# Kernel tuning notes

Hardware: AMD Instinct MI355X
Metric: run time of the kernel (lower is better)

The kernel has to match this reference:

```python
import jax, jax.numpy as jnp
import numpy as np

QMIN, QMAX = 0.0, 255.0  # uint8 affine quantization range


def _quant_dequant(x, scale, zero_point):
    # affine static quantization: q = clamp(round(x/scale) + zp, 0, 255)
    q = jnp.clip(jnp.round(x / scale) + zero_point, QMIN, QMAX)
    # dequantize back to float for the reference GEMM
    return (q - zero_point) * scale


def setup_inputs() -> dict:
    key = jax.random.key(0)
    k1, k2, k3, k4, k5 = jax.random.split(key, 5)
    N, IN, OUT = 4096, 4096, 4096
    x = jax.random.normal(k1, (N, IN), dtype=jnp.float32)
    weight = jax.random.normal(k2, (OUT, IN), dtype=jnp.float32) * 0.02
    bias = jax.random.normal(k3, (OUT,), dtype=jnp.float32)
    # static qparams (as produced by calculate_qparams of the observers)
    act_scale = jnp.float32(4.0 * 2.0 / 255.0)  # covers ~[-4, 4]
    act_zero_point = jnp.int32(128)
    weight_scale = (jax.random.uniform(k4, (OUT,), dtype=jnp.float32) * 0.5 + 0.5) * (0.08 * 2.0 / 255.0)
    weight_zero_point = jnp.full((OUT,), 128, dtype=jnp.int32)
    return {
        "x": x,
        "weight": weight,
        "bias": bias,
        "act_scale": act_scale,
        "act_zero_point": act_zero_point,
        "weight_scale": weight_scale,
        "weight_zero_point": weight_zero_point,
    }


def reference(x, weight, bias, act_scale, act_zero_point, weight_scale, weight_zero_point):
    # per-tensor static activation quantization
    x_dq = _quant_dequant(x, act_scale, act_zero_point.astype(jnp.float32))  # [N, in]
    # per-output-row weight quantization (block_size = (1, in_features))
    w_dq = _quant_dequant(
        weight,
        weight_scale[:, None],
        weight_zero_point.astype(jnp.float32)[:, None],
    )  # [out, in]
    # F.linear: x @ W^T + b
    return jnp.einsum("ni,oi->no", x_dq, w_dq) + bias
```

## Files before the change

kernel.cpp:

```cpp
#include <hip/hip_runtime.h>
#include <stdint.h>

typedef int   int4v   __attribute__((ext_vector_type(4)));
typedef float float4v __attribute__((ext_vector_type(4)));

static constexpr int DIM = 4096;
static constexpr int BM  = 256, BN = 256;
static constexpr int BK  = 128;
static constexpr int NKT = DIM / BK;

__global__ __launch_bounds__(256) void quant_act_kernel(
    const float* __restrict__ x, const float* __restrict__ s_ptr,
    const int* __restrict__ zp_ptr, int* __restrict__ out, int n4) {
  const float s  = s_ptr[0];
  const int   zp = zp_ptr[0];
  int idx    = blockIdx.x * blockDim.x + threadIdx.x;
  int stride = gridDim.x * blockDim.x;
  for (int i = idx; i < n4; i += stride) {
    float4v v = reinterpret_cast<const float4v*>(x)[i];
    int packed = 0;
#pragma unroll
    for (int j = 0; j < 4; ++j) {
      int q = (int)rintf(v[j] / s) + zp;
      q = min(max(q, 0), 255);
      q -= zp;
      packed |= (q & 255) << (8 * j);
    }
    out[i] = packed;
  }
}

__global__ __launch_bounds__(256) void quant_wgt_kernel(
    const float* __restrict__ w, const float* __restrict__ ws,
    const int* __restrict__ wzp, int* __restrict__ out, int n4) {
  int idx    = blockIdx.x * blockDim.x + threadIdx.x;
  int stride = gridDim.x * blockDim.x;
  for (int i = idx; i < n4; i += stride) {
    const int row = i >> 10;
    const float s = ws[row];
    const int  zp = wzp[row];
    float4v v = reinterpret_cast<const float4v*>(w)[i];
    int packed = 0;
#pragma unroll
    for (int j = 0; j < 4; ++j) {
      int q = (int)rintf(v[j] / s) + zp;
      q = min(max(q, 0), 255);
      q -= zp;
      packed |= (q & 255) << (8 * j);
    }
    out[i] = packed;
  }
}


#define PHASE_MFMA(MH, NH)                                                    \
  __builtin_amdgcn_s_barrier();                                               \
  asm volatile("s_waitcnt lgkmcnt(0)" ::: "memory");                          \
  __builtin_amdgcn_s_setprio(1);                                              \
  _Pragma("unroll") for (int kk = 0; kk < 2; ++kk)                            \
  _Pragma("unroll") for (int m = 0; m < 4; ++m)                               \
  _Pragma("unroll") for (int n = 0; n < 2; ++n)                               \
      acc[(MH)*4 + m][(NH)*2 + n] = __builtin_amdgcn_mfma_i32_16x16x64_i8(    \
          af[m][kk], bf[(NH)*2 + n][kk], acc[(MH)*4 + m][(NH)*2 + n], 0,0,0); \
  __builtin_amdgcn_s_setprio(0);                                              \
  __builtin_amdgcn_s_barrier();

__global__ __launch_bounds__(512) void gemm_i8_8ph(
    const signed char* __restrict__ A, const signed char* __restrict__ B,
    const float* __restrict__ s_act, const float* __restrict__ w_scale,
    const float* __restrict__ bias, float* __restrict__ C) {
  extern __shared__ signed char smem[];

  const int tid  = threadIdx.x;
  const int w    = tid >> 6;
  const int lane = tid & 63;
  const int wr = w >> 2, wc = w & 3;
  const int l15 = lane & 15, lhi = lane >> 4;
  const int swk = (l15 & 7) << 4;

  const int srow = lane >> 3;
  const int scol = ((lane & 7) ^ (lane >> 3)) << 4;

  const int bid = blockIdx.x;
  const int swz = (bid & 7) * 32 + (bid >> 3);
  const int tileM = (swz >> 4) * BM;
  const int tileN = (swz & 15) * BN;

  auto stageA = [&](int i, int ktn, signed char* aL) {
    const int c = 4 * w + i;
    const size_t g = (size_t)(tileM + c * 8 + srow) * DIM + (size_t)ktn * BK + scol;
    __builtin_amdgcn_global_load_lds(
        (const __attribute__((address_space(1))) void*)(A + g),
        (__attribute__((address_space(3))) void*)(aL + c * 1024), 16, 0, 0);
  };
  auto stageB = [&](int i, int ktn, signed char* bL) {
    const int c = 4 * w + i;
    const size_t g = (size_t)(tileN + c * 8 + srow) * DIM + (size_t)ktn * BK + scol;
    __builtin_amdgcn_global_load_lds(
        (const __attribute__((address_space(1))) void*)(B + g),
        (__attribute__((address_space(3))) void*)(bL + c * 1024), 16, 0, 0);
  };
  auto rdA = [&](const signed char* aL, int mh, int m, int kk) -> int4v {
    const int r = wr * 128 + (mh * 4 + m) * 16 + l15;
    return *(const int4v*)(aL + r * BK + ((kk * 64 + lhi * 16) ^ swk));
  };
  auto rdB = [&](const signed char* bL, int nidx, int kk) -> int4v {
    const int r = wc * 64 + nidx * 16 + l15;
    return *(const int4v*)(bL + r * BK + ((kk * 64 + lhi * 16) ^ swk));
  };

  int4v acc[8][4] = {};
  int4v af[4][2];
  int4v bf[4][2];

  {
    signed char* a0 = smem;
    signed char* b0 = smem + 32768;
    signed char* a1 = smem + 65536;
    signed char* b1 = smem + 65536 + 32768;
#pragma unroll
    for (int i = 0; i < 4; ++i) { stageA(i, 0, a0); stageB(i, 0, b0); }
#pragma unroll
    for (int i = 0; i < 4; ++i) { stageA(i, 1, a1); stageB(i, 1, b1); }
  }
  asm volatile("s_waitcnt vmcnt(8)" ::: "memory");
  __builtin_amdgcn_s_barrier();

  for (int kt = 0; kt < NKT; ++kt) {
    signed char* aL = smem + (kt & 1) * 65536;
    signed char* bL = aL + 32768;

#pragma unroll
    for (int m = 0; m < 4; ++m) { af[m][0] = rdA(aL, 0, m, 0); af[m][1] = rdA(aL, 0, m, 1); }
#pragma unroll
    for (int n = 0; n < 2; ++n) { bf[n][0] = rdB(bL, n, 0); bf[n][1] = rdB(bL, n, 1); }
    PHASE_MFMA(0, 0)

#pragma unroll
    for (int n = 2; n < 4; ++n) { bf[n][0] = rdB(bL, n, 0); bf[n][1] = rdB(bL, n, 1); }
    PHASE_MFMA(0, 1)

#pragma unroll
    for (int m = 0; m < 4; ++m) { af[m][0] = rdA(aL, 1, m, 0); af[m][1] = rdA(aL, 1, m, 1); }
    PHASE_MFMA(1, 0)

    const bool st = (kt + 2 < NKT);
    if (st) {
#pragma unroll
      for (int i = 0; i < 4; ++i) { stageA(i, kt + 2, aL); stageB(i, kt + 2, bL); }
    }
    __builtin_amdgcn_s_setprio(1);
#pragma unroll
    for (int kk = 0; kk < 2; ++kk)
#pragma unroll
      for (int m = 0; m < 4; ++m)
#pragma unroll
        for (int n = 0; n < 2; ++n)
          acc[4 + m][2 + n] = __builtin_amdgcn_mfma_i32_16x16x64_i8(
              af[m][kk], bf[2 + n][kk], acc[4 + m][2 + n], 0, 0, 0);
    __builtin_amdgcn_s_setprio(0);
    if (st) {
      asm volatile("s_waitcnt vmcnt(8)" ::: "memory");
    } else {
      asm volatile("s_waitcnt vmcnt(0)" ::: "memory");
    }
    __builtin_amdgcn_s_barrier();
  }

  const float sa = s_act[0];
#pragma unroll
  for (int n = 0; n < 4; ++n) {
    const int col = tileN + wc * 64 + n * 16 + l15;
    const float sc = sa * w_scale[col];
    const float bs = bias[col];
#pragma unroll
    for (int m = 0; m < 8; ++m) {
      const int rbase = tileM + wr * 128 + m * 16 + lhi * 4;
#pragma unroll
      for (int j = 0; j < 4; ++j)
        C[(size_t)(rbase + j) * DIM + col] = (float)acc[m][n][j] * sc + bs;
    }
  }
}

extern "C" void kernel_launch(void* const* d_in, const int* in_sizes, int n_in,
                              void* d_out, int out_size, void* d_ws, size_t ws_size,
                              hipStream_t stream) {
  const float* x    = (const float*)d_in[0];
  const float* w    = (const float*)d_in[1];
  const float* bias = (const float*)d_in[2];
  const float* a_s  = (const float*)d_in[3];
  const int*   a_zp = (const int*)d_in[4];
  const float* w_s  = (const float*)d_in[5];
  const int*   w_zp = (const int*)d_in[6];
  float* out = (float*)d_out;

  signed char* a8 = (signed char*)d_ws;
  signed char* b8 = a8 + (size_t)DIM * DIM;

  const int n4 = DIM * DIM / 4;
  quant_act_kernel<<<2048, 256, 0, stream>>>(x, a_s, a_zp, (int*)a8, n4);
  quant_wgt_kernel<<<2048, 256, 0, stream>>>(w, w_s, w_zp, (int*)b8, n4);

  (void)hipFuncSetAttribute((const void*)gemm_i8_8ph,
                            hipFuncAttributeMaxDynamicSharedMemorySize, 131072);
  gemm_i8_8ph<<<256, 512, 131072, stream>>>(a8, b8, a_s, w_s, bias, out);
}
```

Baseline: 99.21 us.

## Software-pipeline LDS fragment reads across k-tiles with split A fragment registers

Restructures the int8 MFMA main loop so that LDS reads for the next phase and the next k-tile's first fragments are issued while the current MFMA quads run, using separate low and high A fragment register sets. It drops the per-phase barriers, keeping two barriers per iteration. The aim is to hide LDS latency behind matrix math and to cut synchronisation stalls. It also replaces the swizzled 1D block mapping with a plain 2D grid, which may change L2 reuse, and the extra fragment registers raise register pressure.

New measurement: 94.74 us. 4.5% less time.

```diff
diff --git a/kernel.cpp b/kernel.cpp
--- a/kernel.cpp
+++ b/kernel.cpp
@@ -53,19 +53,16 @@
 }
 
 
-#define PHASE_MFMA(MH, NH)                                                    \
-  __builtin_amdgcn_s_barrier();                                               \
-  asm volatile("s_waitcnt lgkmcnt(0)" ::: "memory");                          \
-  __builtin_amdgcn_s_setprio(1);                                              \
-  _Pragma("unroll") for (int kk = 0; kk < 2; ++kk)                            \
-  _Pragma("unroll") for (int m = 0; m < 4; ++m)                               \
-  _Pragma("unroll") for (int n = 0; n < 2; ++n)                               \
-      acc[(MH)*4 + m][(NH)*2 + n] = __builtin_amdgcn_mfma_i32_16x16x64_i8(    \
-          af[m][kk], bf[(NH)*2 + n][kk], acc[(MH)*4 + m][(NH)*2 + n], 0,0,0); \
-  __builtin_amdgcn_s_setprio(0);                                              \
-  __builtin_amdgcn_s_barrier();
-
-__global__ __launch_bounds__(512) void gemm_i8_8ph(
+#define MFMA_QUAD(AF, MH, NL)                                                  \
+  __builtin_amdgcn_s_setprio(1);                                               \
+  _Pragma("unroll") for (int kk = 0; kk < 2; ++kk)                             \
+  _Pragma("unroll") for (int m = 0; m < 4; ++m)                                \
+  _Pragma("unroll") for (int n = 0; n < 2; ++n)                                \
+      acc[(MH)*4 + m][(NL) + n] = __builtin_amdgcn_mfma_i32_16x16x64_i8(       \
+          AF[m][kk], bf[(NL) + n][kk], acc[(MH)*4 + m][(NL) + n], 0, 0, 0);    \
+  __builtin_amdgcn_s_setprio(0);
+
+__global__ __launch_bounds__(512) void gemm_i8_pipe(
     const signed char* __restrict__ A, const signed char* __restrict__ B,
     const float* __restrict__ s_act, const float* __restrict__ w_scale,
     const float* __restrict__ bias, float* __restrict__ C) {
@@ -81,10 +78,8 @@
   const int srow = lane >> 3;
   const int scol = ((lane & 7) ^ (lane >> 3)) << 4;
 
-  const int bid = blockIdx.x;
-  const int swz = (bid & 7) * 32 + (bid >> 3);
-  const int tileM = (swz >> 4) * BM;
-  const int tileN = (swz & 15) * BN;
+  const int tileM = blockIdx.y * BM;
+  const int tileN = blockIdx.x * BN;
 
   auto stageA = [&](int i, int ktn, signed char* aL) {
     const int c = 4 * w + i;
@@ -110,7 +105,8 @@
   };
 
   int4v acc[8][4] = {};
-  int4v af[4][2];
+  int4v afLo[4][2];
+  int4v afHi[4][2];
   int4v bf[4][2];
 
   {
@@ -122,49 +118,49 @@
     for (int i = 0; i < 4; ++i) { stageA(i, 0, a0); stageB(i, 0, b0); }
 #pragma unroll
     for (int i = 0; i < 4; ++i) { stageA(i, 1, a1); stageB(i, 1, b1); }
-  }
-  asm volatile("s_waitcnt vmcnt(8)" ::: "memory");
-  __builtin_amdgcn_s_barrier();
+    asm volatile("s_waitcnt vmcnt(8)" ::: "memory");
+    __builtin_amdgcn_s_barrier();
+#pragma unroll
+    for (int m = 0; m < 4; ++m) { afLo[m][0] = rdA(a0, 0, m, 0); afLo[m][1] = rdA(a0, 0, m, 1); }
+#pragma unroll
+    for (int n = 0; n < 2; ++n) { bf[n][0] = rdB(b0, n, 0); bf[n][1] = rdB(b0, n, 1); }
+  }
 
   for (int kt = 0; kt < NKT; ++kt) {
     signed char* aL = smem + (kt & 1) * 65536;
     signed char* bL = aL + 32768;
-
-#pragma unroll
-    for (int m = 0; m < 4; ++m) { af[m][0] = rdA(aL, 0, m, 0); af[m][1] = rdA(aL, 0, m, 1); }
-#pragma unroll
-    for (int n = 0; n < 2; ++n) { bf[n][0] = rdB(bL, n, 0); bf[n][1] = rdB(bL, n, 1); }
-    PHASE_MFMA(0, 0)
+    signed char* aN = smem + ((kt + 1) & 1) * 65536;
+    signed char* bN = aN + 32768;
 
 #pragma unroll
     for (int n = 2; n < 4; ++n) { bf[n][0] = rdB(bL, n, 0); bf[n][1] = rdB(bL, n, 1); }
-    PHASE_MFMA(0, 1)
-
-#pragma unroll
-    for (int m = 0; m < 4; ++m) { af[m][0] = rdA(aL, 1, m, 0); af[m][1] = rdA(aL, 1, m, 1); }
-    PHASE_MFMA(1, 0)
-
-    const bool st = (kt + 2 < NKT);
-    if (st) {
+    MFMA_QUAD(afLo, 0, 0)
+
+#pragma unroll
+    for (int m = 0; m < 4; ++m) { afHi[m][0] = rdA(aL, 1, m, 0); afHi[m][1] = rdA(aL, 1, m, 1); }
+    MFMA_QUAD(afLo, 0, 2)
+    asm volatile("s_waitcnt lgkmcnt(0)" ::: "memory");
+    __builtin_amdgcn_s_barrier();
+
+    if (kt + 2 < NKT) {
 #pragma unroll
       for (int i = 0; i < 4; ++i) { stageA(i, kt + 2, aL); stageB(i, kt + 2, bL); }
     }
-    __builtin_amdgcn_s_setprio(1);
-#pragma unroll
-    for (int kk = 0; kk < 2; ++kk)
-#pragma unroll
-      for (int m = 0; m < 4; ++m)
-#pragma unroll
-        for (int n = 0; n < 2; ++n)
-          acc[4 + m][2 + n] = __builtin_amdgcn_mfma_i32_16x16x64_i8(
-              af[m][kk], bf[2 + n][kk], acc[4 + m][2 + n], 0, 0, 0);
-    __builtin_amdgcn_s_setprio(0);
-    if (st) {
+    MFMA_QUAD(afHi, 1, 0)
+    if (kt + 2 < NKT) {
       asm volatile("s_waitcnt vmcnt(8)" ::: "memory");
     } else {
       asm volatile("s_waitcnt vmcnt(0)" ::: "memory");
     }
     __builtin_amdgcn_s_barrier();
+
+    if (kt + 1 < NKT) {
+#pragma unroll
+      for (int m = 0; m < 4; ++m) { afLo[m][0] = rdA(aN, 0, m, 0); afLo[m][1] = rdA(aN, 0, m, 1); }
+#pragma unroll
+      for (int n = 0; n < 2; ++n) { bf[n][0] = rdB(bN, n, 0); bf[n][1] = rdB(bN, n, 1); }
+    }
+    MFMA_QUAD(afHi, 1, 2)
   }
 
   const float sa = s_act[0];
@@ -202,7 +198,8 @@
   quant_act_kernel<<<2048, 256, 0, stream>>>(x, a_s, a_zp, (int*)a8, n4);
   quant_wgt_kernel<<<2048, 256, 0, stream>>>(w, w_s, w_zp, (int*)b8, n4);
 
-  (void)hipFuncSetAttribute((const void*)gemm_i8_8ph,
+  (void)hipFuncSetAttribute((const void*)gemm_i8_pipe,
                             hipFuncAttributeMaxDynamicSharedMemorySize, 131072);
-  gemm_i8_8ph<<<256, 512, 131072, stream>>>(a8, b8, a_s, w_s, bias, out);
-}
+  dim3 grid(DIM / BN, DIM / BM);
+  gemm_i8_pipe<<<grid, 512, 131072, stream>>>(a8, b8, a_s, w_s, bias, out);
+}
```
